# Performance work log

Hardware: AMD Instinct MI355X
Metric: run time of the kernel (lower is better)

Reference implementation:

```python
import jax, jax.numpy as jnp
import numpy as np

PI = 3.1415926
MAX_V = 8  # max vertices of a quad-quad convex intersection
ALPHA, GAMMA, IOU_THRES = 0.25, 2.0, 0.5


def xyxy2xywh_a(b):
    cx = (b[..., 0] + b[..., 2]) * 0.5
    cy = (b[..., 1] + b[..., 3]) * 0.5
    w = b[..., 2] - b[..., 0]
    h = b[..., 3] - b[..., 1]
    return jnp.stack([cx, cy, w, h, b[..., 4]], -1)


def rbox_2_quad(b):
    # [N,5] (x1,y1,x2,y2,theta_deg) -> [N,4,2] corner quads
    x = xyxy2xywh_a(b)
    cx, cy, w, h, t = x[:, 0], x[:, 1], x[:, 2], x[:, 3], x[:, 4]
    th = t * (PI / 180.0)
    c, s = jnp.cos(th), jnp.sin(th)
    dx = jnp.array([-0.5, 0.5, 0.5, -0.5], b.dtype)
    dy = jnp.array([-0.5, -0.5, 0.5, 0.5], b.dtype)
    px = cx[:, None] + dx * w[:, None] * c[:, None] - dy * h[:, None] * s[:, None]
    py = cy[:, None] + dx * w[:, None] * s[:, None] + dy * h[:, None] * c[:, None]
    return jnp.stack([px, py], -1)


def min_area_square(b):
    cx = (b[:, 0] + b[:, 2]) * 0.5
    cy = (b[:, 1] + b[:, 3]) * 0.5
    s = jnp.maximum(b[:, 2] - b[:, 0], b[:, 3] - b[:, 1]) * 0.5
    return jnp.stack([cx - s, cy - s, cx + s, cy + s], 1)


def bbox_overlaps(a, b):
    # axis-aligned IoU matrix [N,M]
    lt = jnp.maximum(a[:, None, :2], b[None, :, :2])
    rb = jnp.minimum(a[:, None, 2:], b[None, :, 2:])
    wh = jnp.clip(rb - lt, 0.0)
    inter = wh[..., 0] * wh[..., 1]
    area_a = (a[:, 2] - a[:, 0]) * (a[:, 3] - a[:, 1])
    area_b = (b[:, 2] - b[:, 0]) * (b[:, 3] - b[:, 1])
    return inter / (area_a[:, None] + area_b[None, :] - inter + 1e-6)


def points_in_quads(pts, quads):
    # pointsJf: pts [A,2] inside convex quads [G,4,2] -> [A,G] {0,1}
    e = jnp.roll(quads, -1, axis=1) - quads  # [G,4,2]
    rel = pts[:, None, None, :] - quads[None]  # [A,G,4,2]
    cr = e[None, ..., 0] * rel[..., 1] - e[None, ..., 1] * rel[..., 0]
    inside = jnp.all(cr >= 0, -1) | jnp.all(cr <= 0, -1)
    return inside.astype(pts.dtype)


def _signed_area2(q):
    return jnp.sum(q[:, 0] * jnp.roll(q[:, 1], -1) - jnp.roll(q[:, 0], -1) * q[:, 1])


def _quad_inter_area(q1, q2):
    # Sutherland-Hodgman clipping of quad q1 by convex quad q2, fixed 8-vertex buffer
    q1 = jnp.where(_signed_area2(q1) < 0, q1[::-1], q1)
    q2 = jnp.where(_signed_area2(q2) < 0, q2[::-1], q2)
    poly = jnp.zeros((MAX_V, 2), q1.dtype).at[:4].set(q1)
    edges = jnp.stack([q2, jnp.roll(q2, -1, axis=0)], 1)  # [4,2,2]

    def clip(carry, edge):
        poly, n = carry
        a, b = edge[0], edge[1]
        idx = jnp.arange(MAX_V)
        nidx = jnp.where(idx + 1 < n, idx + 1, 0)
        cur, nxt = poly, poly[nidx]
        d = b - a
        dc = d[0] * (cur[:, 1] - a[1]) - d[1] * (cur[:, 0] - a[0])
        dn = d[0] * (nxt[:, 1] - a[1]) - d[1] * (nxt[:, 0] - a[0])
        denom = dc - dn
        t = dc / jnp.where(jnp.abs(denom) < 1e-12, 1e-12, denom)
        inter = cur + t[:, None] * (nxt - cur)
        active = idx < n
        keep_cur = active & (dc >= 0)
        keep_int = active & ((dc >= 0) != (dn >= 0))
        pts = jnp.stack([cur, inter], 1).reshape(2 * MAX_V, 2)
        flags = jnp.stack([keep_cur, keep_int], 1).reshape(-1)
        pos = jnp.where(flags, jnp.cumsum(flags) - 1, MAX_V)
        newpoly = jnp.zeros((MAX_V + 1, 2), poly.dtype).at[pos].set(pts)[:MAX_V]
        return (newpoly, flags.sum()), None

    (poly, n), _ = jax.lax.scan(clip, (poly, jnp.int32(4)), edges)
    idx = jnp.arange(MAX_V)
    nidx = jnp.where(idx + 1 < n, idx + 1, 0)
    contrib = poly[:, 0] * poly[nidx, 1] - poly[nidx, 0] * poly[:, 1]
    area = 0.5 * jnp.abs(jnp.sum(jnp.where(idx < n, contrib, 0.0)))
    return jnp.where(n >= 3, area, 0.0)


def rbox_overlaps(quads_a, quads_g, gate, thresh=0.1):
    area_a = 0.5 * jnp.abs(jax.vmap(_signed_area2)(quads_a))
    area_g = 0.5 * jnp.abs(jax.vmap(_signed_area2)(quads_g))
    inter = jax.vmap(lambda qa: jax.vmap(lambda qg: _quad_inter_area(qa, qg))(quads_g))(quads_a)
    iou = inter / (area_a[:, None] + area_g[None, :] - inter + 1e-6)
    return jnp.where(gate > thresh, iou, 0.0)


def encode(anchors, gt):
    a = xyxy2xywh_a(anchors)
    g = xyxy2xywh_a(gt)
    dx = (g[:, 0] - a[:, 0]) / a[:, 2]
    dy = (g[:, 1] - a[:, 1]) / a[:, 3]
    dw = jnp.log(g[:, 2] / a[:, 2])
    dh = jnp.log(g[:, 3] / a[:, 3])
    dt = (g[:, 4] - a[:, 4]) * (PI / 180.0)
    return jnp.stack([dx, dy, dw, dh, dt], 1)


def decode(anchors, deltas):
    a = xyxy2xywh_a(anchors)
    cx = a[..., 0] + deltas[..., 0] * a[..., 2]
    cy = a[..., 1] + deltas[..., 1] * a[..., 3]
    w = a[..., 2] * jnp.exp(deltas[..., 2])
    h = a[..., 3] * jnp.exp(deltas[..., 3])
    t = a[..., 4] + deltas[..., 4] * (180.0 / PI)
    return jnp.stack([cx, cy, w, h, t], -1)


def smooth_l1(x, t, beta=1.0 / 9):
    diff = jnp.abs(x - t)
    return jnp.where(diff < beta, 0.5 * diff * diff / beta, diff - 0.5 * beta)


def _forward(classifications, regressions, anchors, annotations):
    B = classifications.shape[0]
    _ = decode(anchors, regressions)  # all_pred_boxes (unused when func='smooth')
    cls_losses, reg_losses = [], []
    for j in range(B):
        cls = jnp.clip(classifications[j], 1e-4, 1.0 - 1e-4)
        anch = anchors[j]
        gtb = annotations[j, :, :5]
        labels = annotations[j, :, 5].astype(jnp.int32)
        indicator = bbox_overlaps(min_area_square(anch), min_area_square(gtb))
        centers = xyxy2xywh_a(anch)[:, :2]
        quads_g = rbox_2_quad(gtb)
        inside = points_in_quads(centers, quads_g)
        quads_a = rbox_2_quad(anch)
        ious = rbox_overlaps(quads_a, quads_g, inside * indicator)  # [A,G]
        iou_max = ious.max(1)
        iou_argmax = ious.argmax(1)
        pos = iou_max >= IOU_THRES
        max_gt = ious.max(0)
        argmax_gt = ious.argmax(0)
        low = (max_gt < IOU_THRES).astype(jnp.int32)
        pos = (pos.astype(jnp.int32).at[argmax_gt].max(low)).astype(bool)
        num_pos = pos.sum()
        C = cls.shape[1]
        onehot = jax.nn.one_hot(labels[iou_argmax], C, dtype=cls.dtype)
        tgt = -jnp.ones_like(cls)
        tgt = jnp.where((iou_max < IOU_THRES - 0.1)[:, None], 0.0, tgt)
        tgt = jnp.where(pos[:, None], onehot, tgt)
        af = jnp.where(tgt == 1.0, ALPHA, 1.0 - ALPHA)
        fw = af * jnp.where(tgt == 1.0, 1.0 - cls, cls) ** GAMMA
        bce = -(tgt * jnp.log(cls + 1e-6) + (1.0 - tgt) * jnp.log(1.0 - cls + 1e-6))
        cls_loss = jnp.where(tgt != -1.0, fw * bce, 0.0).sum() / jnp.maximum(num_pos.astype(cls.dtype), 1.0)
        cls_losses.append(cls_loss)
        reg_t = encode(anch, gtb[iou_argmax])
        l = smooth_l1(regressions[j], reg_t)
        denom = (jnp.maximum(num_pos, 1) * l.shape[1]).astype(l.dtype)
        reg_loss = jnp.where(num_pos > 0, (l * pos[:, None].astype(l.dtype)).sum() / denom, 0.0)
        reg_losses.append(reg_loss)
    loss_cls = 5.0 * jnp.stack(cls_losses).mean(keepdims=True)
    loss_reg = 2.0 * jnp.stack(reg_losses).mean(keepdims=True)
    return loss_cls, loss_reg


def setup_inputs() -> dict:
    key = jax.random.key(0)
    ks = jax.random.split(key, 8)
    B, A, G, C = 2, 32768, 32, 15
    cls = jax.random.uniform(ks[0], (B, A, C), jnp.float32)
    reg = jax.random.normal(ks[1], (B, A, 5), jnp.float32) * 0.1
    ac = jax.random.uniform(ks[2], (B, A, 2), jnp.float32, 0.0, 1024.0)
    awh = jax.random.uniform(ks[3], (B, A, 2), jnp.float32, 16.0, 256.0)
    anchors = jnp.concatenate([ac - awh * 0.5, ac + awh * 0.5, jnp.zeros((B, A, 1), jnp.float32)], -1)
    gc = jax.random.uniform(ks[4], (B, G, 2), jnp.float32, 64.0, 960.0)
    gwh = jax.random.uniform(ks[5], (B, G, 2), jnp.float32, 24.0, 300.0)
    gt = jax.random.uniform(ks[6], (B, G, 1), jnp.float32, -90.0, 90.0)
    glab = jax.random.randint(ks[7], (B, G, 1), 0, C).astype(jnp.float32)
    annotations = jnp.concatenate([gc - gwh * 0.5, gc + gwh * 0.5, gt, glab], -1)
    return {"classifications": cls, "regressions": reg, "anchors": anchors, "annotations": annotations}


def reference(classifications, regressions, anchors, annotations):
    return _forward(classifications, regressions, anchors, annotations)
```

## Files before the change

### kernel.cpp

```cpp
#include <hip/hip_runtime.h>

#define A_N 32768
#define G_N 32
#define C_N 15
#define BPB 128
#define DEG2RAD ((float)(3.1415926 / 180.0))
#define BETA (1.0f / 9.0f)

typedef unsigned long long ull;

template <int NIN>
__device__ __forceinline__ int clip_pass(float ax, float ay, float dx, float dy,
                                         float (&PX)[8], float (&PY)[8], int n) {
  constexpr int NOUT = (NIN + 1 < 8) ? NIN + 1 : 8;
  float d[NIN];
#pragma unroll
  for (int i = 0; i < NIN; ++i)
    d[i] = dx * (PY[i] - ay) - dy * (PX[i] - ax);
  float NX[NOUT], NY[NOUT];
#pragma unroll
  for (int i = 0; i < NOUT; ++i) { NX[i] = 0.f; NY[i] = 0.f; }
  int m = 0;
#pragma unroll
  for (int i = 0; i < NIN; ++i) {
    if (i < n) {
      bool w = (i + 1 < n);
      float dn = w ? d[(i + 1) % NIN] : d[0];
      float xn = w ? PX[(i + 1) % NIN] : PX[0];
      float yn = w ? PY[(i + 1) % NIN] : PY[0];
      bool kc = (d[i] >= 0.f);
      bool kn = (dn >= 0.f);
      if (kc) {
#pragma unroll
        for (int o = 0; o < NOUT; ++o)
          if (o <= 2 * i && m == o) { NX[o] = PX[i]; NY[o] = PY[i]; }
        ++m;
      }
      if (kc != kn) {
        float den = d[i] - dn;
        if (fabsf(den) < 1e-12f) den = 1e-12f;
        float t = d[i] / den;
        float ix = PX[i] + t * (xn - PX[i]);
        float iy = PY[i] + t * (yn - PY[i]);
#pragma unroll
        for (int o = 0; o < NOUT; ++o)
          if (o <= 2 * i + 1 && m == o) { NX[o] = ix; NY[o] = iy; }
        ++m;
      }
    }
  }
#pragma unroll
  for (int i = 0; i < NOUT; ++i) { PX[i] = NX[i]; PY[i] = NY[i]; }
#pragma unroll
  for (int i = NOUT; i < 8; ++i) { PX[i] = 0.f; PY[i] = 0.f; }
  return m;
}

__global__ __launch_bounds__(256) void k_main(
    const float* __restrict__ anchors, const float* __restrict__ annot,
    float* __restrict__ iou_max, int* __restrict__ iou_arg,
    int* __restrict__ posf, ull* __restrict__ gpart, unsigned* done) {
  int j = blockIdx.x >> 7;
  int blk = blockIdx.x & (BPB - 1);
  int tid = threadIdx.x;
  int a = blk * 256 + tid;

  if (blockIdx.x == 0 && tid == 0)
    __hip_atomic_store(done, 0u, __ATOMIC_RELAXED, __HIP_MEMORY_SCOPE_AGENT);

  __shared__ float g_qx[G_N][4], g_qy[G_N][4];
  __shared__ float g_sq[G_N][4];
  __shared__ float g_sarea[G_N], g_qarea[G_N];
  __shared__ float a_q[256][8];
  __shared__ float a_area[256];
  __shared__ ull rowbest[256];
  __shared__ ull colmax[G_N];
  __shared__ unsigned short list[256 * G_N];
  __shared__ int cnt;

  if (tid == 0) cnt = 0;
  rowbest[tid] = 0xFFFFFFFFull;
  if (tid < G_N) colmax[tid] = 0xFFFFFFFFull;

  if (tid < G_N) {
    const float* g = annot + ((size_t)j * G_N + tid) * 6;
    float x1 = g[0], y1 = g[1], x2 = g[2], y2 = g[3], t = g[4];
    float cxx = (x1 + x2) * 0.5f, cyy = (y1 + y2) * 0.5f;
    float w = x2 - x1, h = y2 - y1;
    float th = t * DEG2RAD;
    float c = cosf(th), s = sinf(th);
    const float ddx[4] = {-0.5f, 0.5f, 0.5f, -0.5f};
    const float ddy[4] = {-0.5f, -0.5f, 0.5f, 0.5f};
    float px[4], py[4];
#pragma unroll
    for (int k = 0; k < 4; ++k) {
      px[k] = cxx + ddx[k] * w * c - ddy[k] * h * s;
      py[k] = cyy + ddx[k] * w * s + ddy[k] * h * c;
    }
    float s2 = 0.f;
#pragma unroll
    for (int k = 0; k < 4; ++k)
      s2 += px[k] * py[(k + 1) & 3] - px[(k + 1) & 3] * py[k];
    if (s2 < 0.f) {
#pragma unroll
      for (int k = 0; k < 4; ++k) { g_qx[tid][k] = px[3 - k]; g_qy[tid][k] = py[3 - k]; }
    } else {
#pragma unroll
      for (int k = 0; k < 4; ++k) { g_qx[tid][k] = px[k]; g_qy[tid][k] = py[k]; }
    }
    g_qarea[tid] = 0.5f * fabsf(s2);
    float half = fmaxf(w, h) * 0.5f;
    float sx1 = cxx - half, sy1 = cyy - half, sx2 = cxx + half, sy2 = cyy + half;
    g_sq[tid][0] = sx1; g_sq[tid][1] = sy1; g_sq[tid][2] = sx2; g_sq[tid][3] = sy2;
    g_sarea[tid] = (sx2 - sx1) * (sy2 - sy1);
  }

  const float* an = anchors + ((size_t)j * A_N + a) * 5;
  float ax1 = an[0], ay1 = an[1], ax2 = an[2], ay2 = an[3], at = an[4];
  float acx = (ax1 + ax2) * 0.5f, acy = (ay1 + ay2) * 0.5f;
  float aw = ax2 - ax1, ah = ay2 - ay1;
  float ath = at * DEG2RAD;
  float ac = cosf(ath), asn = sinf(ath);
  {
    const float ddx[4] = {-0.5f, 0.5f, 0.5f, -0.5f};
    const float ddy[4] = {-0.5f, -0.5f, 0.5f, 0.5f};
    float apx[4], apy[4];
#pragma unroll
    for (int k = 0; k < 4; ++k) {
      apx[k] = acx + ddx[k] * aw * ac - ddy[k] * ah * asn;
      apy[k] = acy + ddx[k] * aw * asn + ddy[k] * ah * ac;
    }
    float s2a = 0.f;
#pragma unroll
    for (int k = 0; k < 4; ++k)
      s2a += apx[k] * apy[(k + 1) & 3] - apx[(k + 1) & 3] * apy[k];
    if (s2a < 0.f) {
      float tx = apx[0], ty = apy[0];
      apx[0] = apx[3]; apy[0] = apy[3]; apx[3] = tx; apy[3] = ty;
      tx = apx[1]; ty = apy[1];
      apx[1] = apx[2]; apy[1] = apy[2]; apx[2] = tx; apy[2] = ty;
    }
#pragma unroll
    for (int k = 0; k < 4; ++k) { a_q[tid][k] = apx[k]; a_q[tid][4 + k] = apy[k]; }
    a_area[tid] = 0.5f * fabsf(s2a);
  }
  float half = fmaxf(aw, ah) * 0.5f;
  float asx1 = acx - half, asy1 = acy - half, asx2 = acx + half, asy2 = acy + half;
  float asarea = (asx2 - asx1) * (asy2 - asy1);
  __syncthreads();

  for (int g = 0; g < G_N; ++g) {
    float ltx = fmaxf(asx1, g_sq[g][0]);
    float lty = fmaxf(asy1, g_sq[g][1]);
    float rbx = fminf(asx2, g_sq[g][2]);
    float rby = fminf(asy2, g_sq[g][3]);
    float iw = fmaxf(rbx - ltx, 0.f);
    float ih = fmaxf(rby - lty, 0.f);
    float inter_s = iw * ih;
    float ind = inter_s / (asarea + g_sarea[g] - inter_s + 1e-6f);
    bool pall = true, nall = true;
#pragma unroll
    for (int k = 0; k < 4; ++k) {
      float ex = g_qx[g][(k + 1) & 3] - g_qx[g][k];
      float ey = g_qy[g][(k + 1) & 3] - g_qy[g][k];
      float rx = acx - g_qx[g][k];
      float ry = acy - g_qy[g][k];
      float cr = ex * ry - ey * rx;
      pall = pall && (cr >= 0.f);
      nall = nall && (cr <= 0.f);
    }
    if ((pall || nall) && ind > 0.1f) {
      int p = atomicAdd(&cnt, 1);
      list[p] = (unsigned short)((tid << 5) | g);
    }
  }
  __syncthreads();

  int np = cnt;
  for (int i = tid; i < np; i += 256) {
    int ent = list[i];
    int la = ent >> 5, g = ent & 31;
    float PX[8], PY[8];
#pragma unroll
    for (int k = 0; k < 4; ++k) { PX[k] = a_q[la][k]; PY[k] = a_q[la][4 + k]; }
#pragma unroll
    for (int k = 4; k < 8; ++k) { PX[k] = 0.f; PY[k] = 0.f; }
    float gx0 = g_qx[g][0], gy0 = g_qy[g][0];
    float gx1 = g_qx[g][1], gy1 = g_qy[g][1];
    float gx2 = g_qx[g][2], gy2 = g_qy[g][2];
    float gx3 = g_qx[g][3], gy3 = g_qy[g][3];
    int n = 4;
    n = clip_pass<4>(gx0, gy0, gx1 - gx0, gy1 - gy0, PX, PY, n);
    n = clip_pass<5>(gx1, gy1, gx2 - gx1, gy2 - gy1, PX, PY, n);
    n = clip_pass<6>(gx2, gy2, gx3 - gx2, gy3 - gy2, PX, PY, n);
    n = clip_pass<7>(gx3, gy3, gx0 - gx3, gy0 - gy3, PX, PY, n);
    float s = 0.f;
#pragma unroll
    for (int k = 0; k < 8; ++k) {
      if (k < n) {
        float xn = (k + 1 < n) ? PX[(k + 1) & 7] : PX[0];
        float yn = (k + 1 < n) ? PY[(k + 1) & 7] : PY[0];
        s += PX[k] * yn - xn * PY[k];
      }
    }
    float inter = (n >= 3) ? 0.5f * fabsf(s) : 0.f;
    float v = inter / (a_area[la] + g_qarea[g] - inter + 1e-6f);
    ull pr = ((ull)__float_as_uint(v) << 32) | (unsigned)(~(unsigned)g);
    atomicMax(&rowbest[la], pr);
    unsigned ga = (unsigned)(blk * 256 + la);
    ull pc = ((ull)__float_as_uint(v) << 32) | (unsigned)(~ga);
    atomicMax(&colmax[g], pc);
  }
  __syncthreads();

  size_t ia = (size_t)j * A_N + a;
  ull rb = rowbest[tid];
  float best = __uint_as_float((unsigned)(rb >> 32));
  int barg = (int)(~(unsigned)rb);
  iou_max[ia] = best;
  iou_arg[ia] = barg;
  posf[ia] = (best >= 0.5f) ? 1 : 0;
  if (tid < G_N)
    gpart[((size_t)j * BPB + blk) * G_N + tid] = colmax[tid];
}

__global__ __launch_bounds__(256) void k_loss(
    const float* __restrict__ cls_in, const float* __restrict__ reg_in,
    const float* __restrict__ anchors, const float* __restrict__ annot,
    const float* __restrict__ iou_max, const int* __restrict__ iou_arg,
    const int* __restrict__ posf, const ull* __restrict__ gpart,
    float* __restrict__ cls_part, float* __restrict__ reg_part,
    int* __restrict__ cnt_part, unsigned* done, float* __restrict__ out, int B) {
  int j = blockIdx.x >> 7;
  int blk = blockIdx.x & (BPB - 1);
  int tid = threadIdx.x;
  int a = blk * 256 + tid;
  (void)blk;

  __shared__ int lab[G_N];
  __shared__ float gcx[G_N], gcy[G_N], gw[G_N], gh[G_N], gth[G_N];
  __shared__ ull sred[8][G_N];
  __shared__ int forced[G_N];

  {
    int g = tid & 31, chunk = tid >> 5;
    const ull* gp = gpart + (size_t)j * BPB * G_N;
    ull m = 0;
#pragma unroll
    for (int b = 0; b < BPB / 8; ++b) {
      ull v = gp[(size_t)(chunk * (BPB / 8) + b) * G_N + g];
      m = v > m ? v : m;
    }
    sred[chunk][g] = m;
  }
  if (tid < G_N) {
    const float* g = annot + ((size_t)j * G_N + tid) * 6;
    gcx[tid] = (g[0] + g[2]) * 0.5f;
    gcy[tid] = (g[1] + g[3]) * 0.5f;
    gw[tid] = g[2] - g[0];
    gh[tid] = g[3] - g[1];
    gth[tid] = g[4];
    lab[tid] = (int)g[5];
  }
  __syncthreads();
  if (tid < G_N) {
    ull m = sred[0][tid];
#pragma unroll
    for (int c = 1; c < 8; ++c) m = sred[c][tid] > m ? sred[c][tid] : m;
    float v = __uint_as_float((unsigned)(m >> 32));
    forced[tid] = (v < 0.5f) ? (int)(~(unsigned)m) : -1;
  }
  __syncthreads();

  size_t ia = (size_t)j * A_N + a;
  float im = iou_max[ia];
  int arg = iou_arg[ia];
  int p = posf[ia];
#pragma unroll
  for (int g2 = 0; g2 < G_N; ++g2)
    if (forced[g2] == a) p = 1;
  int lb = lab[arg];
  const float* c = cls_in + ia * C_N;

  float pcv[C_N];
#pragma unroll
  for (int ci = 0; ci < C_N; ++ci) pcv[ci] = c[ci];

  float csum = 0.f;
  bool bg = (im < 0.4f);
  if (p || bg) {
#pragma unroll
    for (int ci = 0; ci < C_N; ++ci) {
      float pc = fminf(fmaxf(pcv[ci], 1e-4f), 0.9999f);
      bool tgt1 = p && (ci == lb);
      if (tgt1)
        csum += 0.25f * (1.f - pc) * (1.f - pc) * (-__logf(pc + 1e-6f));
      else
        csum += 0.75f * pc * pc * (-__logf(1.f - pc + 1e-6f));
    }
  }

  float rsum = 0.f;
  if (p) {
    const float* an = anchors + ia * 5;
    float ax1 = an[0], ay1 = an[1], ax2 = an[2], ay2 = an[3], at = an[4];
    float acx = (ax1 + ax2) * 0.5f, acy = (ay1 + ay2) * 0.5f;
    float aw = ax2 - ax1, ah = ay2 - ay1;
    const float* r = reg_in + ia * 5;
    float t5[5];
    t5[0] = (gcx[arg] - acx) / aw;
    t5[1] = (gcy[arg] - acy) / ah;
    t5[2] = __logf(gw[arg] / aw);
    t5[3] = __logf(gh[arg] / ah);
    t5[4] = (gth[arg] - at) * DEG2RAD;
#pragma unroll
    for (int i = 0; i < 5; ++i) {
      float d = fabsf(r[i] - t5[i]);
      rsum += (d < BETA) ? (0.5f * d * d / BETA) : (d - 0.5f * BETA);
    }
  }

  __shared__ float s1[256], s2[256];
  __shared__ int s3[256];
  s1[tid] = csum; s2[tid] = rsum; s3[tid] = p;
  __syncthreads();
  for (int o = 128; o; o >>= 1) {
    if (tid < o) { s1[tid] += s1[tid + o]; s2[tid] += s2[tid + o]; s3[tid] += s3[tid + o]; }
    __syncthreads();
  }

  __shared__ int amLast;
  if (tid == 0) {
    __hip_atomic_store(&cls_part[blockIdx.x], s1[0], __ATOMIC_RELAXED, __HIP_MEMORY_SCOPE_AGENT);
    __hip_atomic_store(&reg_part[blockIdx.x], s2[0], __ATOMIC_RELAXED, __HIP_MEMORY_SCOPE_AGENT);
    __hip_atomic_store(&cnt_part[blockIdx.x], s3[0], __ATOMIC_RELAXED, __HIP_MEMORY_SCOPE_AGENT);
    __threadfence();
    unsigned old = __hip_atomic_fetch_add(done, 1u, __ATOMIC_ACQ_REL, __HIP_MEMORY_SCOPE_AGENT);
    amLast = (old == (unsigned)(gridDim.x - 1)) ? 1 : 0;
  }
  __syncthreads();

  if (amLast) {
    int P = (int)gridDim.x;
    float cv = 0.f, rv = 0.f;
    int nv = 0;
    if (tid < P) {
      cv = __hip_atomic_load(&cls_part[tid], __ATOMIC_RELAXED, __HIP_MEMORY_SCOPE_AGENT);
      rv = __hip_atomic_load(&reg_part[tid], __ATOMIC_RELAXED, __HIP_MEMORY_SCOPE_AGENT);
      nv = __hip_atomic_load(&cnt_part[tid], __ATOMIC_RELAXED, __HIP_MEMORY_SCOPE_AGENT);
    }
    __syncthreads();
    s1[tid] = cv; s2[tid] = rv; s3[tid] = nv;
    __syncthreads();
    for (int o = 64; o; o >>= 1) {
      if ((tid & 127) < o) {
        s1[tid] += s1[tid + o]; s2[tid] += s2[tid + o]; s3[tid] += s3[tid + o];
      }
      __syncthreads();
    }
    if (tid == 0) {
      float cl = 0.f, rl = 0.f;
      for (int jj = 0; jj < B; ++jj) {
        float cs = s1[jj * 128], rs = s2[jj * 128];
        int np = s3[jj * 128];
        float npf = (np > 0) ? (float)np : 1.f;
        cl += cs / npf;
        rl += (np > 0) ? rs / (npf * 5.f) : 0.f;
      }
      out[0] = 5.0f * cl / (float)B;
      out[1] = 2.0f * rl / (float)B;
    }
  }
}

extern "C" void kernel_launch(void* const* d_in, const int* in_sizes, int n_in,
                              void* d_out, int out_size, void* d_ws, size_t ws_size,
                              hipStream_t stream) {
  const float* cls = (const float*)d_in[0];
  const float* reg = (const float*)d_in[1];
  const float* anc = (const float*)d_in[2];
  const float* ann = (const float*)d_in[3];
  int B = in_sizes[3] / (G_N * 6);

  char* w = (char*)d_ws;
  unsigned* done = (unsigned*)w;  w += 64;
  ull* gpart = (ull*)w;           w += (size_t)B * BPB * G_N * sizeof(ull);
  float* iou_max = (float*)w;     w += (size_t)B * A_N * 4;
  int* iou_arg = (int*)w;         w += (size_t)B * A_N * 4;
  int* posf = (int*)w;            w += (size_t)B * A_N * 4;
  float* cls_part = (float*)w;    w += (size_t)B * BPB * 4;
  float* reg_part = (float*)w;    w += (size_t)B * BPB * 4;
  int* cnt_part = (int*)w;        w += (size_t)B * BPB * 4;

  k_main<<<B * BPB, 256, 0, stream>>>(anc, ann, iou_max, iou_arg, posf, gpart, done);
  k_loss<<<B * BPB, 256, 0, stream>>>(cls, reg, anc, ann, iou_max, iou_arg, posf,
                                      gpart, cls_part, reg_part, cnt_part, done,
                                      (float*)d_out, B);
}
```

Before: 37.36 us.

## Fuse IoU and loss kernels into one cooperative kernel with grid syncs

Merges the IoU/matching kernel and the loss kernel into a single cooperative launch that uses grid.sync() in place of the second kernel boundary and the last-block atomic counter. Per-anchor IoU max, argmax and positive flags now stay in registers rather than going through global memory, and classification and regression inputs are loaded early so their latency overlaps the IoU work. Shared-memory GT and anchor quads are repacked into float4 vectors. The trade-off is two grid-wide barriers, a cooperative launch that needs all 256 blocks resident at once, and more register and shared-memory pressure per block.

```diff
diff --git a/kernel.cpp b/kernel.cpp
--- a/kernel.cpp
+++ b/kernel.cpp
@@ -1,4 +1,7 @@
 #include <hip/hip_runtime.h>
+#include <hip/hip_cooperative_groups.h>
+
+namespace cg = cooperative_groups;
 
 #define A_N 32768
 #define G_N 32
@@ -56,27 +59,47 @@
   return m;
 }
 
-__global__ __launch_bounds__(256) void k_main(
+__global__ __launch_bounds__(256) void k_fused(
+    const float* __restrict__ cls_in, const float* __restrict__ reg_in,
     const float* __restrict__ anchors, const float* __restrict__ annot,
-    float* __restrict__ iou_max, int* __restrict__ iou_arg,
-    int* __restrict__ posf, ull* __restrict__ gpart, unsigned* done) {
+    ull* __restrict__ gpart, float* __restrict__ cls_part,
+    float* __restrict__ reg_part, int* __restrict__ cnt_part,
+    float* __restrict__ out, int B) {
+  cg::grid_group grid = cg::this_grid();
   int j = blockIdx.x >> 7;
   int blk = blockIdx.x & (BPB - 1);
   int tid = threadIdx.x;
   int a = blk * 256 + tid;
-
-  if (blockIdx.x == 0 && tid == 0)
-    __hip_atomic_store(done, 0u, __ATOMIC_RELAXED, __HIP_MEMORY_SCOPE_AGENT);
-
-  __shared__ float g_qx[G_N][4], g_qy[G_N][4];
-  __shared__ float g_sq[G_N][4];
-  __shared__ float g_sarea[G_N], g_qarea[G_N];
-  __shared__ float a_q[256][8];
+  size_t ia = (size_t)j * A_N + a;
+
+  __shared__ float4 g_sqv[G_N];
+  __shared__ float2 g_meta[G_N];
+  __shared__ float4 g_vx[G_N], g_vy[G_N];
+  __shared__ float4 a_qx[256], a_qy[256];
   __shared__ float a_area[256];
   __shared__ ull rowbest[256];
   __shared__ ull colmax[G_N];
   __shared__ unsigned short list[256 * G_N];
   __shared__ int cnt;
+  __shared__ int lab[G_N];
+  __shared__ float gcx[G_N], gcy[G_N], gw2[G_N], gh2[G_N], gth[G_N];
+  __shared__ ull sred[8][G_N];
+  __shared__ int forced[G_N];
+  __shared__ float s1[256], s2[256];
+  __shared__ int s3[256];
+
+  float pcv[C_N];
+  {
+    const float* c = cls_in + ia * C_N;
+#pragma unroll
+    for (int ci = 0; ci < C_N; ++ci) pcv[ci] = c[ci];
+  }
+  float rv[5];
+  {
+    const float* r = reg_in + ia * 5;
+#pragma unroll
+    for (int i = 0; i < 5; ++i) rv[i] = r[i];
+  }
 
   if (tid == 0) cnt = 0;
   rowbest[tid] = 0xFFFFFFFFull;
@@ -87,6 +110,8 @@
     float x1 = g[0], y1 = g[1], x2 = g[2], y2 = g[3], t = g[4];
     float cxx = (x1 + x2) * 0.5f, cyy = (y1 + y2) * 0.5f;
     float w = x2 - x1, h = y2 - y1;
+    gcx[tid] = cxx; gcy[tid] = cyy; gw2[tid] = w; gh2[tid] = h; gth[tid] = t;
+    lab[tid] = (int)g[5];
     float th = t * DEG2RAD;
     float c = cosf(th), s = sinf(th);
     const float ddx[4] = {-0.5f, 0.5f, 0.5f, -0.5f};
@@ -102,25 +127,25 @@
     for (int k = 0; k < 4; ++k)
       s2 += px[k] * py[(k + 1) & 3] - px[(k + 1) & 3] * py[k];
     if (s2 < 0.f) {
-#pragma unroll
-      for (int k = 0; k < 4; ++k) { g_qx[tid][k] = px[3 - k]; g_qy[tid][k] = py[3 - k]; }
+      g_vx[tid] = make_float4(px[3], px[2], px[1], px[0]);
+      g_vy[tid] = make_float4(py[3], py[2], py[1], py[0]);
     } else {
-#pragma unroll
-      for (int k = 0; k < 4; ++k) { g_qx[tid][k] = px[k]; g_qy[tid][k] = py[k]; }
-    }
-    g_qarea[tid] = 0.5f * fabsf(s2);
+      g_vx[tid] = make_float4(px[0], px[1], px[2], px[3]);
+      g_vy[tid] = make_float4(py[0], py[1], py[2], py[3]);
+    }
     float half = fmaxf(w, h) * 0.5f;
     float sx1 = cxx - half, sy1 = cyy - half, sx2 = cxx + half, sy2 = cyy + half;
-    g_sq[tid][0] = sx1; g_sq[tid][1] = sy1; g_sq[tid][2] = sx2; g_sq[tid][3] = sy2;
-    g_sarea[tid] = (sx2 - sx1) * (sy2 - sy1);
-  }
-
-  const float* an = anchors + ((size_t)j * A_N + a) * 5;
+    g_sqv[tid] = make_float4(sx1, sy1, sx2, sy2);
+    g_meta[tid] = make_float2((sx2 - sx1) * (sy2 - sy1), 0.5f * fabsf(s2));
+  }
+
+  const float* an = anchors + ia * 5;
   float ax1 = an[0], ay1 = an[1], ax2 = an[2], ay2 = an[3], at = an[4];
   float acx = (ax1 + ax2) * 0.5f, acy = (ay1 + ay2) * 0.5f;
   float aw = ax2 - ax1, ah = ay2 - ay1;
   float ath = at * DEG2RAD;
   float ac = cosf(ath), asn = sinf(ath);
+  float my_area;
   {
     const float ddx[4] = {-0.5f, 0.5f, 0.5f, -0.5f};
     const float ddy[4] = {-0.5f, -0.5f, 0.5f, 0.5f};
@@ -140,35 +165,35 @@
       tx = apx[1]; ty = apy[1];
       apx[1] = apx[2]; apy[1] = apy[2]; apx[2] = tx; apy[2] = ty;
     }
-#pragma unroll
-    for (int k = 0; k < 4; ++k) { a_q[tid][k] = apx[k]; a_q[tid][4 + k] = apy[k]; }
-    a_area[tid] = 0.5f * fabsf(s2a);
+    a_qx[tid] = make_float4(apx[0], apx[1], apx[2], apx[3]);
+    a_qy[tid] = make_float4(apy[0], apy[1], apy[2], apy[3]);
+    my_area = 0.5f * fabsf(s2a);
+    a_area[tid] = my_area;
   }
   float half = fmaxf(aw, ah) * 0.5f;
   float asx1 = acx - half, asy1 = acy - half, asx2 = acx + half, asy2 = acy + half;
   float asarea = (asx2 - asx1) * (asy2 - asy1);
   __syncthreads();
 
+#pragma unroll 2
   for (int g = 0; g < G_N; ++g) {
-    float ltx = fmaxf(asx1, g_sq[g][0]);
-    float lty = fmaxf(asy1, g_sq[g][1]);
-    float rbx = fminf(asx2, g_sq[g][2]);
-    float rby = fminf(asy2, g_sq[g][3]);
+    float4 sq = g_sqv[g];
+    float2 meta = g_meta[g];
+    float ltx = fmaxf(asx1, sq.x);
+    float lty = fmaxf(asy1, sq.y);
+    float rbx = fminf(asx2, sq.z);
+    float rby = fminf(asy2, sq.w);
     float iw = fmaxf(rbx - ltx, 0.f);
     float ih = fmaxf(rby - lty, 0.f);
     float inter_s = iw * ih;
-    float ind = inter_s / (asarea + g_sarea[g] - inter_s + 1e-6f);
-    bool pall = true, nall = true;
-#pragma unroll
-    for (int k = 0; k < 4; ++k) {
-      float ex = g_qx[g][(k + 1) & 3] - g_qx[g][k];
-      float ey = g_qy[g][(k + 1) & 3] - g_qy[g][k];
-      float rx = acx - g_qx[g][k];
-      float ry = acy - g_qy[g][k];
-      float cr = ex * ry - ey * rx;
-      pall = pall && (cr >= 0.f);
-      nall = nall && (cr <= 0.f);
-    }
+    float ind = inter_s / (asarea + meta.x - inter_s + 1e-6f);
+    float4 vx = g_vx[g], vy = g_vy[g];
+    float cr0 = (vx.y - vx.x) * (acy - vy.x) - (vy.y - vy.x) * (acx - vx.x);
+    float cr1 = (vx.z - vx.y) * (acy - vy.y) - (vy.z - vy.y) * (acx - vx.y);
+    float cr2 = (vx.w - vx.z) * (acy - vy.z) - (vy.w - vy.z) * (acx - vx.z);
+    float cr3 = (vx.x - vx.w) * (acy - vy.w) - (vy.x - vy.w) * (acx - vx.w);
+    bool pall = (cr0 >= 0.f) & (cr1 >= 0.f) & (cr2 >= 0.f) & (cr3 >= 0.f);
+    bool nall = (cr0 <= 0.f) & (cr1 <= 0.f) & (cr2 <= 0.f) & (cr3 <= 0.f);
     if ((pall || nall) && ind > 0.1f) {
       int p = atomicAdd(&cnt, 1);
       list[p] = (unsigned short)((tid << 5) | g);
@@ -180,20 +205,18 @@
   for (int i = tid; i < np; i += 256) {
     int ent = list[i];
     int la = ent >> 5, g = ent & 31;
+    float4 aqx = a_qx[la], aqy = a_qy[la];
     float PX[8], PY[8];
-#pragma unroll
-    for (int k = 0; k < 4; ++k) { PX[k] = a_q[la][k]; PY[k] = a_q[la][4 + k]; }
+    PX[0] = aqx.x; PX[1] = aqx.y; PX[2] = aqx.z; PX[3] = aqx.w;
+    PY[0] = aqy.x; PY[1] = aqy.y; PY[2] = aqy.z; PY[3] = aqy.w;
 #pragma unroll
     for (int k = 4; k < 8; ++k) { PX[k] = 0.f; PY[k] = 0.f; }
-    float gx0 = g_qx[g][0], gy0 = g_qy[g][0];
-    float gx1 = g_qx[g][1], gy1 = g_qy[g][1];
-    float gx2 = g_qx[g][2], gy2 = g_qy[g][2];
-    float gx3 = g_qx[g][3], gy3 = g_qy[g][3];
+    float4 gvx = g_vx[g], gvy = g_vy[g];
     int n = 4;
-    n = clip_pass<4>(gx0, gy0, gx1 - gx0, gy1 - gy0, PX, PY, n);
-    n = clip_pass<5>(gx1, gy1, gx2 - gx1, gy2 - gy1, PX, PY, n);
-    n = clip_pass<6>(gx2, gy2, gx3 - gx2, gy3 - gy2, PX, PY, n);
-    n = clip_pass<7>(gx3, gy3, gx0 - gx3, gy0 - gy3, PX, PY, n);
+    n = clip_pass<4>(gvx.x, gvy.x, gvx.y - gvx.x, gvy.y - gvy.x, PX, PY, n);
+    n = clip_pass<5>(gvx.y, gvy.y, gvx.z - gvx.y, gvy.z - gvy.y, PX, PY, n);
+    n = clip_pass<6>(gvx.z, gvy.z, gvx.w - gvx.z, gvy.w - gvy.z, PX, PY, n);
+    n = clip_pass<7>(gvx.w, gvy.w, gvx.x - gvx.w, gvy.x - gvy.w, PX, PY, n);
     float s = 0.f;
 #pragma unroll
     for (int k = 0; k < 8; ++k) {
@@ -204,7 +227,7 @@
       }
     }
     float inter = (n >= 3) ? 0.5f * fabsf(s) : 0.f;
-    float v = inter / (a_area[la] + g_qarea[g] - inter + 1e-6f);
+    float v = inter / (a_area[la] + g_meta[g].y - inter + 1e-6f);
     ull pr = ((ull)__float_as_uint(v) << 32) | (unsigned)(~(unsigned)g);
     atomicMax(&rowbest[la], pr);
     unsigned ga = (unsigned)(blk * 256 + la);
@@ -213,34 +236,16 @@
   }
   __syncthreads();
 
-  size_t ia = (size_t)j * A_N + a;
   ull rb = rowbest[tid];
-  float best = __uint_as_float((unsigned)(rb >> 32));
-  int barg = (int)(~(unsigned)rb);
-  iou_max[ia] = best;
-  iou_arg[ia] = barg;
-  posf[ia] = (best >= 0.5f) ? 1 : 0;
+  float im = __uint_as_float((unsigned)(rb >> 32));
+  int arg = (int)(~(unsigned)rb);
+  int p = (im >= 0.5f) ? 1 : 0;
+
   if (tid < G_N)
-    gpart[((size_t)j * BPB + blk) * G_N + tid] = colmax[tid];
-}
-
-__global__ __launch_bounds__(256) void k_loss(
-    const float* __restrict__ cls_in, const float* __restrict__ reg_in,
-    const float* __restrict__ anchors, const float* __restrict__ annot,
-    const float* __restrict__ iou_max, const int* __restrict__ iou_arg,
-    const int* __restrict__ posf, const ull* __restrict__ gpart,
-    float* __restrict__ cls_part, float* __restrict__ reg_part,
-    int* __restrict__ cnt_part, unsigned* done, float* __restrict__ out, int B) {
-  int j = blockIdx.x >> 7;
-  int blk = blockIdx.x & (BPB - 1);
-  int tid = threadIdx.x;
-  int a = blk * 256 + tid;
-  (void)blk;
-
-  __shared__ int lab[G_N];
-  __shared__ float gcx[G_N], gcy[G_N], gw[G_N], gh[G_N], gth[G_N];
-  __shared__ ull sred[8][G_N];
-  __shared__ int forced[G_N];
+    __hip_atomic_store(&gpart[((size_t)j * BPB + blk) * G_N + tid], colmax[tid],
+                       __ATOMIC_RELAXED, __HIP_MEMORY_SCOPE_AGENT);
+  __threadfence();
+  grid.sync();
 
   {
     int g = tid & 31, chunk = tid >> 5;
@@ -248,19 +253,11 @@
     ull m = 0;
 #pragma unroll
     for (int b = 0; b < BPB / 8; ++b) {
-      ull v = gp[(size_t)(chunk * (BPB / 8) + b) * G_N + g];
+      ull v = __hip_atomic_load(&gp[(size_t)(chunk * (BPB / 8) + b) * G_N + g],
+                                __ATOMIC_RELAXED, __HIP_MEMORY_SCOPE_AGENT);
       m = v > m ? v : m;
     }
     sred[chunk][g] = m;
-  }
-  if (tid < G_N) {
-    const float* g = annot + ((size_t)j * G_N + tid) * 6;
-    gcx[tid] = (g[0] + g[2]) * 0.5f;
-    gcy[tid] = (g[1] + g[3]) * 0.5f;
-    gw[tid] = g[2] - g[0];
-    gh[tid] = g[3] - g[1];
-    gth[tid] = g[4];
-    lab[tid] = (int)g[5];
   }
   __syncthreads();
   if (tid < G_N) {
@@ -272,19 +269,10 @@
   }
   __syncthreads();
 
-  size_t ia = (size_t)j * A_N + a;
-  float im = iou_max[ia];
-  int arg = iou_arg[ia];
-  int p = posf[ia];
 #pragma unroll
   for (int g2 = 0; g2 < G_N; ++g2)
     if (forced[g2] == a) p = 1;
   int lb = lab[arg];
-  const float* c = cls_in + ia * C_N;
-
-  float pcv[C_N];
-#pragma unroll
-  for (int ci = 0; ci < C_N; ++ci) pcv[ci] = c[ci];
 
   float csum = 0.f;
   bool bg = (im < 0.4f);
@@ -302,55 +290,44 @@
 
   float rsum = 0.f;
   if (p) {
-    const float* an = anchors + ia * 5;
-    float ax1 = an[0], ay1 = an[1], ax2 = an[2], ay2 = an[3], at = an[4];
-    float acx = (ax1 + ax2) * 0.5f, acy = (ay1 + ay2) * 0.5f;
-    float aw = ax2 - ax1, ah = ay2 - ay1;
-    const float* r = reg_in + ia * 5;
     float t5[5];
     t5[0] = (gcx[arg] - acx) / aw;
     t5[1] = (gcy[arg] - acy) / ah;
-    t5[2] = __logf(gw[arg] / aw);
-    t5[3] = __logf(gh[arg] / ah);
+    t5[2] = __logf(gw2[arg] / aw);
+    t5[3] = __logf(gh2[arg] / ah);
     t5[4] = (gth[arg] - at) * DEG2RAD;
 #pragma unroll
     for (int i = 0; i < 5; ++i) {
-      float d = fabsf(r[i] - t5[i]);
+      float d = fabsf(rv[i] - t5[i]);
       rsum += (d < BETA) ? (0.5f * d * d / BETA) : (d - 0.5f * BETA);
     }
   }
 
-  __shared__ float s1[256], s2[256];
-  __shared__ int s3[256];
   s1[tid] = csum; s2[tid] = rsum; s3[tid] = p;
   __syncthreads();
   for (int o = 128; o; o >>= 1) {
     if (tid < o) { s1[tid] += s1[tid + o]; s2[tid] += s2[tid + o]; s3[tid] += s3[tid + o]; }
     __syncthreads();
   }
-
-  __shared__ int amLast;
   if (tid == 0) {
     __hip_atomic_store(&cls_part[blockIdx.x], s1[0], __ATOMIC_RELAXED, __HIP_MEMORY_SCOPE_AGENT);
     __hip_atomic_store(&reg_part[blockIdx.x], s2[0], __ATOMIC_RELAXED, __HIP_MEMORY_SCOPE_AGENT);
     __hip_atomic_store(&cnt_part[blockIdx.x], s3[0], __ATOMIC_RELAXED, __HIP_MEMORY_SCOPE_AGENT);
-    __threadfence();
-    unsigned old = __hip_atomic_fetch_add(done, 1u, __ATOMIC_ACQ_REL, __HIP_MEMORY_SCOPE_AGENT);
-    amLast = (old == (unsigned)(gridDim.x - 1)) ? 1 : 0;
-  }
-  __syncthreads();
-
-  if (amLast) {
+  }
+  __threadfence();
+  grid.sync();
+
+  if (blockIdx.x == 0) {
     int P = (int)gridDim.x;
-    float cv = 0.f, rv = 0.f;
+    float cv = 0.f, rvv = 0.f;
     int nv = 0;
     if (tid < P) {
       cv = __hip_atomic_load(&cls_part[tid], __ATOMIC_RELAXED, __HIP_MEMORY_SCOPE_AGENT);
-      rv = __hip_atomic_load(&reg_part[tid], __ATOMIC_RELAXED, __HIP_MEMORY_SCOPE_AGENT);
+      rvv = __hip_atomic_load(&reg_part[tid], __ATOMIC_RELAXED, __HIP_MEMORY_SCOPE_AGENT);
       nv = __hip_atomic_load(&cnt_part[tid], __ATOMIC_RELAXED, __HIP_MEMORY_SCOPE_AGENT);
     }
     __syncthreads();
-    s1[tid] = cv; s2[tid] = rv; s3[tid] = nv;
+    s1[tid] = cv; s2[tid] = rvv; s3[tid] = nv;
     __syncthreads();
     for (int o = 64; o; o >>= 1) {
       if ((tid & 127) < o) {
@@ -362,10 +339,10 @@
       float cl = 0.f, rl = 0.f;
       for (int jj = 0; jj < B; ++jj) {
         float cs = s1[jj * 128], rs = s2[jj * 128];
-        int np = s3[jj * 128];
-        float npf = (np > 0) ? (float)np : 1.f;
+        int npn = s3[jj * 128];
+        float npf = (npn > 0) ? (float)npn : 1.f;
         cl += cs / npf;
-        rl += (np > 0) ? rs / (npf * 5.f) : 0.f;
+        rl += (npn > 0) ? rs / (npf * 5.f) : 0.f;
       }
       out[0] = 5.0f * cl / (float)B;
       out[1] = 2.0f * rl / (float)B;
@@ -383,17 +360,15 @@
   int B = in_sizes[3] / (G_N * 6);
 
   char* w = (char*)d_ws;
-  unsigned* done = (unsigned*)w;  w += 64;
   ull* gpart = (ull*)w;           w += (size_t)B * BPB * G_N * sizeof(ull);
-  float* iou_max = (float*)w;     w += (size_t)B * A_N * 4;
-  int* iou_arg = (int*)w;         w += (size_t)B * A_N * 4;
-  int* posf = (int*)w;            w += (size_t)B * A_N * 4;
   float* cls_part = (float*)w;    w += (size_t)B * BPB * 4;
   float* reg_part = (float*)w;    w += (size_t)B * BPB * 4;
   int* cnt_part = (int*)w;        w += (size_t)B * BPB * 4;
-
-  k_main<<<B * BPB, 256, 0, stream>>>(anc, ann, iou_max, iou_arg, posf, gpart, done);
-  k_loss<<<B * BPB, 256, 0, stream>>>(cls, reg, anc, ann, iou_max, iou_arg, posf,
-                                      gpart, cls_part, reg_part, cnt_part, done,
-                                      (float*)d_out, B);
+  float* outp = (float*)d_out;
+
+  void* args[] = {(void*)&cls, (void*)&reg, (void*)&anc, (void*)&ann,
+                  (void*)&gpart, (void*)&cls_part, (void*)&reg_part,
+                  (void*)&cnt_part, (void*)&outp, (void*)&B};
+  hipLaunchCooperativeKernel((const void*)k_fused, dim3(B * BPB), dim3(256),
+                             args, 0, stream);
 }
```

New measurement: 135.0 us. 261% more time.
